# Performance work log

Hardware: AMD Instinct MI355X
Metric: run time of the kernel (lower is better)

The kernel has to match this reference:

```python
import jax, jax.numpy as jnp
import numpy as np

D_MODEL = 256
D_AUDIO = 256
W2V_DIM = 768
LIB_DIM = 93
N_LAYERS = 4
D_STATE = 16
D_CONV = 4
EXPAND = 2
D_INNER = EXPAND * D_MODEL  # 512
DT_RANK = (D_MODEL + 15) // 16  # 16
B, L = 8, 1024


def _silu(x):
    return x * jax.nn.sigmoid(x)


def _layernorm(x, g, b):
    mu = jnp.mean(x, axis=-1, keepdims=True)
    var = jnp.mean((x - mu) ** 2, axis=-1, keepdims=True)
    return (x - mu) * jax.lax.rsqrt(var + 1e-5) * g + b


def _mamba(x, in_W, conv_W, conv_b, xproj_W, dt_W, dt_b, A_log, D_vec, out_W):
    # x: [B, L, d_model]
    xz = jnp.einsum('bld,ed->ble', x, in_W)          # [B, L, 2*d_inner]
    xc, z = jnp.split(xz, 2, axis=-1)
    # causal depthwise conv1d over time
    u = jnp.swapaxes(xc, 1, 2)                        # [B, d_inner, L]
    u = jax.lax.conv_general_dilated(
        u, conv_W[:, None, :], (1,), [(D_CONV - 1, 0)],
        dimension_numbers=('NCH', 'OIH', 'NCH'), feature_group_count=D_INNER)
    xc = _silu(jnp.swapaxes(u, 1, 2) + conv_b)        # [B, L, d_inner]
    dbl = jnp.einsum('bld,ed->ble', xc, xproj_W)      # [B, L, dt_rank+2*d_state]
    dt, Bm, Cm = jnp.split(dbl, [DT_RANK, DT_RANK + D_STATE], axis=-1)
    dt = jax.nn.softplus(jnp.einsum('blr,dr->bld', dt, dt_W) + dt_b)  # [B, L, d_inner]
    A = -jnp.exp(A_log)                               # [d_inner, d_state]

    def step(h, inp):
        dt_t, x_t, B_t, C_t = inp                     # [B,d_inner],[B,d_inner],[B,S],[B,S]
        dA = jnp.exp(dt_t[..., None] * A)             # [B, d_inner, S]
        h = h * dA + (dt_t * x_t)[..., None] * B_t[:, None, :]
        y = jnp.einsum('bds,bs->bd', h, C_t)
        return h, y

    h0 = jnp.zeros((x.shape[0], D_INNER, D_STATE), x.dtype)
    xs = (jnp.swapaxes(dt, 0, 1), jnp.swapaxes(xc, 0, 1),
          jnp.swapaxes(Bm, 0, 1), jnp.swapaxes(Cm, 0, 1))
    _, ys = jax.lax.scan(step, h0, xs)                # ys: [L, B, d_inner]
    y = jnp.swapaxes(ys, 0, 1) + xc * D_vec
    y = y * _silu(z)
    return jnp.einsum('bld,ed->ble', y, out_W)


def setup_inputs() -> dict:
    key = jax.random.key(0)
    ks = jax.random.split(key, 24)

    def g(k, shape, scale):
        return (jax.random.normal(k, shape, dtype=jnp.float32) * scale)

    inp = {}
    inp['wav2vec_feat'] = jax.random.normal(ks[0], (B, L, W2V_DIM), dtype=jnp.float32)
    inp['librosa_feat'] = jax.random.normal(ks[1], (B, L, LIB_DIM), dtype=jnp.float32)
    inp['w2v_W'] = g(ks[2], (D_AUDIO, W2V_DIM), W2V_DIM ** -0.5)
    inp['w2v_b'] = jnp.zeros((D_AUDIO,), jnp.float32)
    inp['lib_W'] = g(ks[3], (D_AUDIO, LIB_DIM), LIB_DIM ** -0.5)
    inp['lib_b'] = jnp.zeros((D_AUDIO,), jnp.float32)
    inp['fuse_W'] = g(ks[4], (D_MODEL, 2 * D_AUDIO), (2 * D_AUDIO) ** -0.5)
    inp['fuse_b'] = jnp.zeros((D_MODEL,), jnp.float32)
    inp['proj_W'] = g(ks[5], (D_MODEL, D_MODEL), D_MODEL ** -0.5)
    inp['proj_b'] = jnp.zeros((D_MODEL,), jnp.float32)
    # stacked per-layer Mamba params, leading dim = N_LAYERS
    inp['ln_g'] = jnp.ones((N_LAYERS, D_MODEL), jnp.float32)
    inp['ln_b'] = jnp.zeros((N_LAYERS, D_MODEL), jnp.float32)
    inp['in_W'] = g(ks[6], (N_LAYERS, 2 * D_INNER, D_MODEL), D_MODEL ** -0.5)
    inp['conv_W'] = g(ks[7], (N_LAYERS, D_INNER, D_CONV), D_CONV ** -0.5)
    inp['conv_b'] = jnp.zeros((N_LAYERS, D_INNER), jnp.float32)
    inp['xproj_W'] = g(ks[8], (N_LAYERS, DT_RANK + 2 * D_STATE, D_INNER), D_INNER ** -0.5)
    inp['dt_W'] = g(ks[9], (N_LAYERS, D_INNER, DT_RANK), DT_RANK ** -0.5)
    inp['dt_b'] = jnp.full((N_LAYERS, D_INNER), -4.6, jnp.float32)  # softplus -> ~0.01
    A0 = jnp.log(jnp.arange(1, D_STATE + 1, dtype=jnp.float32))
    inp['A_log'] = jnp.broadcast_to(A0, (N_LAYERS, D_INNER, D_STATE)).copy()
    inp['D_vec'] = jnp.ones((N_LAYERS, D_INNER), jnp.float32)
    inp['out_W'] = g(ks[10], (N_LAYERS, D_MODEL, D_INNER), D_INNER ** -0.5)
    inp['fnorm_g'] = jnp.ones((D_MODEL,), jnp.float32)
    inp['fnorm_b'] = jnp.zeros((D_MODEL,), jnp.float32)
    return inp


def reference(wav2vec_feat, librosa_feat, w2v_W, w2v_b, lib_W, lib_b,
              fuse_W, fuse_b, proj_W, proj_b, ln_g, ln_b, in_W, conv_W, conv_b,
              xproj_W, dt_W, dt_b, A_log, D_vec, out_W, fnorm_g, fnorm_b):
    w = jnp.einsum('bld,ed->ble', wav2vec_feat, w2v_W) + w2v_b
    l = jnp.einsum('bld,ed->ble', librosa_feat, lib_W) + lib_b
    h = jnp.einsum('bld,ed->ble', jnp.concatenate([w, l], axis=-1), fuse_W) + fuse_b
    # MambaEncoder: proj -> blocks -> final norm
    h = jnp.einsum('bld,ed->ble', h, proj_W) + proj_b
    for i in range(N_LAYERS):
        h = h + _mamba(_layernorm(h, ln_g[i], ln_b[i]), in_W[i], conv_W[i],
                       conv_b[i], xproj_W[i], dt_W[i], dt_b[i], A_log[i],
                       D_vec[i], out_W[i])
    return _layernorm(h, fnorm_g, fnorm_b)
```

## Files before the change

kernel.cpp:

```cpp
#include <hip/hip_runtime.h>
#include <math.h>


#define CH 64
#define CT 16

typedef __attribute__((ext_vector_type(8))) short bfrag8;
typedef __attribute__((ext_vector_type(4))) float floatx4;

__device__ __forceinline__ float silu_f(float x) { return x / (1.f + __expf(-x)); }
__device__ __forceinline__ unsigned short f2bf(float x) {
    union { float f; unsigned int u; } c; c.f = x;
    unsigned int r = (c.u + 0x7fffu + ((c.u >> 16) & 1u)) >> 16;
    return (unsigned short)r;
}
__device__ __forceinline__ float bf2f(unsigned short u) {
    union { unsigned int u; float f; } c; c.u = ((unsigned int)u) << 16; return c.f;
}
__device__ __forceinline__ floatx4 exp4(floatx4 x) {
    floatx4 r;
    r[0] = __expf(x[0]); r[1] = __expf(x[1]); r[2] = __expf(x[2]); r[3] = __expf(x[3]);
    return r;
}

#define NJOBS 10
struct CvtJobs {
    const float* src[NJOBS];
    unsigned short* dst[NJOBS];
    int n_src[NJOBS];
    int n_tot[NJOBS];
    int start_blk[NJOBS + 1];
};
__global__ void conv_bf16_multi(CvtJobs J)
{
    int blk = blockIdx.x;
    int job = 0;
    while (job + 1 < NJOBS && blk >= J.start_blk[job + 1]) job++;
    int i = (blk - J.start_blk[job]) * 1024 + threadIdx.x * 4;
    if (i >= J.n_tot[job]) return;
    const float* src = J.src[job];
    unsigned short* dst = J.dst[job];
    int ns = J.n_src[job];
    if (i + 3 < ns) {
        float4 v = *(const float4*)(src + i);
        dst[i] = f2bf(v.x); dst[i+1] = f2bf(v.y); dst[i+2] = f2bf(v.z); dst[i+3] = f2bf(v.w);
    } else {
#pragma unroll
        for (int j = 0; j < 4; j++) dst[i+j] = (i+j < ns) ? f2bf(src[i+j]) : (unsigned short)0;
    }
}

__global__ void pad_bf16_kernel(const float* __restrict__ src, unsigned short* __restrict__ dst,
                                int rows, int cs, int cd)
{
    int i = blockIdx.x * 256 + threadIdx.x;
    if (i >= rows * cd) return;
    int row = i / cd, c = i - row * cd;
    dst[i] = (c < cs) ? f2bf(src[row * cs + c]) : (unsigned short)0;
}

template<int RM, int RN>
__global__ __launch_bounds__(64)
void dmfma_gemm(const unsigned short* __restrict__ A, int lda,
                const unsigned short* __restrict__ W, int ldw,
                int K, const float* __restrict__ bias, const float* __restrict__ Cin,
                float* __restrict__ Cf32, unsigned short* __restrict__ Cbf16,
                int N, int ldc, int act)
{
    int lane = threadIdx.x;
    int lm = lane & 15, qk = lane >> 4;
    int m0 = blockIdx.y * (16 * RM);
    int n0 = blockIdx.x * (16 * RN);

    const unsigned short* Ab = A + (size_t)(m0 + lm) * lda + qk * 8;
    const unsigned short* Wb = W + (size_t)(n0 + lm) * ldw + qk * 8;

    floatx4 acc[RM][RN];
#pragma unroll
    for (int i = 0; i < RM; i++)
#pragma unroll
        for (int j = 0; j < RN; j++) acc[i][j] = (floatx4){0.f, 0.f, 0.f, 0.f};

    bfrag8 af[RM], wf[RN];
#pragma unroll
    for (int i = 0; i < RM; i++) af[i] = *(const bfrag8*)(Ab + (size_t)i * 16 * lda);
#pragma unroll
    for (int j = 0; j < RN; j++) wf[j] = *(const bfrag8*)(Wb + (size_t)j * 16 * ldw);

    for (int k0 = 32; k0 < K; k0 += 32) {
        bfrag8 afn[RM], wfn[RN];
#pragma unroll
        for (int i = 0; i < RM; i++) afn[i] = *(const bfrag8*)(Ab + (size_t)i * 16 * lda + k0);
#pragma unroll
        for (int j = 0; j < RN; j++) wfn[j] = *(const bfrag8*)(Wb + (size_t)j * 16 * ldw + k0);
#pragma unroll
        for (int i = 0; i < RM; i++)
#pragma unroll
            for (int j = 0; j < RN; j++)
                acc[i][j] = __builtin_amdgcn_mfma_f32_16x16x32_bf16(af[i], wf[j], acc[i][j], 0, 0, 0);
#pragma unroll
        for (int i = 0; i < RM; i++) af[i] = afn[i];
#pragma unroll
        for (int j = 0; j < RN; j++) wf[j] = wfn[j];
    }
#pragma unroll
    for (int i = 0; i < RM; i++)
#pragma unroll
        for (int j = 0; j < RN; j++)
            acc[i][j] = __builtin_amdgcn_mfma_f32_16x16x32_bf16(af[i], wf[j], acc[i][j], 0, 0, 0);

#pragma unroll
    for (int i = 0; i < RM; i++) {
        int mrow = m0 + i * 16 + qk * 4;
#pragma unroll
        for (int j = 0; j < RN; j++) {
            int n = n0 + j * 16 + lm;
            if (n < N) {
#pragma unroll
                for (int r = 0; r < 4; r++) {
                    float v = acc[i][j][r];
                    size_t o = (size_t)(mrow + r) * ldc + n;
                    if (bias) v += bias[n];
                    if (act == 1) v = fmaxf(v, 0.f) + log1pf(__expf(-fabsf(v)));
                    if (Cin) v += Cin[o];
                    if (Cf32) Cf32[o] = v;
                    if (Cbf16) Cbf16[o] = f2bf(v);
                }
            }
        }
    }
}

__global__ void ln_kernel(const float* __restrict__ x, const float* __restrict__ g,
                          const float* __restrict__ b, float* __restrict__ yf,
                          unsigned short* __restrict__ ybf)
{
    int row = blockIdx.x * 4 + (threadIdx.x >> 6);
    int lane = threadIdx.x & 63;
    size_t o = (size_t)row * 256 + lane * 4;
    floatx4 v = *(const floatx4*)(x + o);
    float s1 = v[0] + v[1] + v[2] + v[3];
    float s2 = v[0]*v[0] + v[1]*v[1] + v[2]*v[2] + v[3]*v[3];
#pragma unroll
    for (int off = 1; off < 64; off <<= 1) {
        s1 += __shfl_xor(s1, off);
        s2 += __shfl_xor(s2, off);
    }
    float mu = s1 * (1.f / 256.f);
    float var = s2 * (1.f / 256.f) - mu * mu;
    float rs = rsqrtf(var + 1e-5f);
    floatx4 gv = *(const floatx4*)(g + lane * 4);
    floatx4 bv = *(const floatx4*)(b + lane * 4);
    floatx4 out = (v - mu) * rs * gv + bv;
    if (yf) *(floatx4*)(yf + o) = out;
    if (ybf) {
        ushort4 pk;
        pk.x = f2bf(out[0]); pk.y = f2bf(out[1]); pk.z = f2bf(out[2]); pk.w = f2bf(out[3]);
        *(ushort4*)(ybf + o) = pk;
    }
}

__global__ void conv_silu_kernel(const unsigned short* __restrict__ xz, const float* __restrict__ cw,
                                 const float* __restrict__ cb, unsigned short* __restrict__ xc)
{
    int idx = blockIdx.x * 256 + threadIdx.x;
    int d4 = (idx & 127) << 2;
    int bt = idx >> 7;
    int t = bt & 1023;
    floatx4 acc = *(const floatx4*)(cb + d4);
    floatx4 w0 = *(const floatx4*)(cw + d4 * 4);
    floatx4 w1 = *(const floatx4*)(cw + d4 * 4 + 4);
    floatx4 w2 = *(const floatx4*)(cw + d4 * 4 + 8);
    floatx4 w3 = *(const floatx4*)(cw + d4 * 4 + 12);
#pragma unroll
    for (int j = 0; j < 4; j++) {
        int tt = t + j - 3;
        if (tt >= 0) {
            ushort4 v = *(const ushort4*)(xz + (size_t)(bt + j - 3) * 1024 + d4);
            acc[0] += bf2f(v.x) * w0[j];
            acc[1] += bf2f(v.y) * w1[j];
            acc[2] += bf2f(v.z) * w2[j];
            acc[3] += bf2f(v.w) * w3[j];
        }
    }
    ushort4 o;
    o.x = f2bf(silu_f(acc[0])); o.y = f2bf(silu_f(acc[1]));
    o.z = f2bf(silu_f(acc[2])); o.w = f2bf(silu_f(acc[3]));
    *(ushort4*)(xc + (size_t)bt * 512 + d4) = o;
}

__global__ __launch_bounds__(256, 4)
void scan_chunk_kernel(const unsigned short* __restrict__ xc, const float* __restrict__ dbl,
                       const unsigned short* __restrict__ dtb, const float* __restrict__ A_log,
                       float* __restrict__ dtsums, float* __restrict__ Hbuf)
{
    int bi = blockIdx.x;
    int dgrp = bi & 1;
    int chunk = (bi >> 1) & (CH - 1);
    int b = bi >> 7;
    int d = dgrp * 256 + threadIdx.x;

    floatx4 a0 = -exp4(*(const floatx4*)(A_log + d * 16));
    floatx4 a1 = -exp4(*(const floatx4*)(A_log + d * 16 + 4));
    floatx4 a2 = -exp4(*(const floatx4*)(A_log + d * 16 + 8));
    floatx4 a3 = -exp4(*(const floatx4*)(A_log + d * 16 + 12));

    floatx4 z4 = (floatx4){0.f, 0.f, 0.f, 0.f};
    floatx4 h0 = z4, h1 = z4, h2 = z4, h3 = z4;
    float dtsum = 0.f;

    size_t rbt = (size_t)b * 1024 + chunk * CT;
    float dt_v = bf2f(dtb[rbt * 512 + d]);
    float x_v  = bf2f(xc[rbt * 512 + d]);
    const float* row = dbl + rbt * 48;
    floatx4 B0 = *(const floatx4*)(row + 16);
    floatx4 B1 = *(const floatx4*)(row + 20);
    floatx4 B2 = *(const floatx4*)(row + 24);
    floatx4 B3 = *(const floatx4*)(row + 28);

    for (int t = 0; t < CT - 1; t++) {
        size_t r2 = rbt + 1;
        float dt_n = bf2f(dtb[r2 * 512 + d]);
        float x_n  = bf2f(xc[r2 * 512 + d]);
        const float* rown = dbl + r2 * 48;
        floatx4 Bn0 = *(const floatx4*)(rown + 16);
        floatx4 Bn1 = *(const floatx4*)(rown + 20);
        floatx4 Bn2 = *(const floatx4*)(rown + 24);
        floatx4 Bn3 = *(const floatx4*)(rown + 28);

        float dtx = dt_v * x_v;
        dtsum += dt_v;
        floatx4 dA;
        dA = exp4(dt_v * a0); h0 = h0 * dA + dtx * B0;
        dA = exp4(dt_v * a1); h1 = h1 * dA + dtx * B1;
        dA = exp4(dt_v * a2); h2 = h2 * dA + dtx * B2;
        dA = exp4(dt_v * a3); h3 = h3 * dA + dtx * B3;

        dt_v = dt_n; x_v = x_n;
        B0 = Bn0; B1 = Bn1; B2 = Bn2; B3 = Bn3;
        rbt = r2;
    }
    {
        float dtx = dt_v * x_v;
        dtsum += dt_v;
        floatx4 dA;
        dA = exp4(dt_v * a0); h0 = h0 * dA + dtx * B0;
        dA = exp4(dt_v * a1); h1 = h1 * dA + dtx * B1;
        dA = exp4(dt_v * a2); h2 = h2 * dA + dtx * B2;
        dA = exp4(dt_v * a3); h3 = h3 * dA + dtx * B3;
    }
    size_t base = (size_t)chunk * 65536 + ((b * 512 + d) * 16);
    *(floatx4*)&Hbuf[base]      = h0;
    *(floatx4*)&Hbuf[base + 4]  = h1;
    *(floatx4*)&Hbuf[base + 8]  = h2;
    *(floatx4*)&Hbuf[base + 12] = h3;
    dtsums[chunk * 4096 + b * 512 + d] = dtsum;
}

__global__ void scan_carry_kernel(const float* __restrict__ dtsums, const float* __restrict__ A_log,
                                  float* __restrict__ Hbuf)
{
    int ch = blockIdx.x * 256 + threadIdx.x;
    int s = ch & 15;
    int bd = ch >> 4;
    int d = bd & 511;
    float a = -__expf(A_log[d * 16 + s]);
    float h = 0.f;
#pragma unroll 8
    for (int c = 0; c < CH; c++) {
        float hl = Hbuf[(size_t)c * 65536 + ch];
        float P = __expf(dtsums[c * 4096 + bd] * a);
        Hbuf[(size_t)c * 65536 + ch] = h;
        h = fmaf(P, h, hl);
    }
}

__global__ __launch_bounds__(256, 4)
void scan_final_kernel(const unsigned short* __restrict__ xc, const float* __restrict__ dbl,
                       const unsigned short* __restrict__ dtb, const unsigned short* __restrict__ xz,
                       const float* __restrict__ A_log, const float* __restrict__ Dvec,
                       const float* __restrict__ Hbuf, unsigned short* __restrict__ y)
{
    int bi = blockIdx.x;
    int dgrp = bi & 1;
    int chunk = (bi >> 1) & (CH - 1);
    int b = bi >> 7;
    int d = dgrp * 256 + threadIdx.x;

    floatx4 a0 = -exp4(*(const floatx4*)(A_log + d * 16));
    floatx4 a1 = -exp4(*(const floatx4*)(A_log + d * 16 + 4));
    floatx4 a2 = -exp4(*(const floatx4*)(A_log + d * 16 + 8));
    floatx4 a3 = -exp4(*(const floatx4*)(A_log + d * 16 + 12));
    float dcoef = Dvec[d];

    size_t base = (size_t)chunk * 65536 + ((b * 512 + d) * 16);
    floatx4 h0 = *(const floatx4*)&Hbuf[base];
    floatx4 h1 = *(const floatx4*)&Hbuf[base + 4];
    floatx4 h2 = *(const floatx4*)&Hbuf[base + 8];
    floatx4 h3 = *(const floatx4*)&Hbuf[base + 12];

    size_t rbt = (size_t)b * 1024 + chunk * CT;
    float dt_v = bf2f(dtb[rbt * 512 + d]);
    float x_v  = bf2f(xc[rbt * 512 + d]);
    float z_v  = bf2f(xz[rbt * 1024 + 512 + d]);
    const float* row = dbl + rbt * 48;
    floatx4 B0 = *(const floatx4*)(row + 16);
    floatx4 B1 = *(const floatx4*)(row + 20);
    floatx4 B2 = *(const floatx4*)(row + 24);
    floatx4 B3 = *(const floatx4*)(row + 28);

    for (int t = 0; t < CT - 1; t++) {
        size_t r2 = rbt + 1;
        float dt_n = bf2f(dtb[r2 * 512 + d]);
        float x_n  = bf2f(xc[r2 * 512 + d]);
        float z_n  = bf2f(xz[r2 * 1024 + 512 + d]);
        const float* rown = dbl + r2 * 48;
        floatx4 Bn0 = *(const floatx4*)(rown + 16);
        floatx4 Bn1 = *(const floatx4*)(rown + 20);
        floatx4 Bn2 = *(const floatx4*)(rown + 24);
        floatx4 Bn3 = *(const floatx4*)(rown + 28);

        float dtx = dt_v * x_v;
        floatx4 dA;
        dA = exp4(dt_v * a0); h0 = h0 * dA + dtx * B0;
        dA = exp4(dt_v * a1); h1 = h1 * dA + dtx * B1;
        dA = exp4(dt_v * a2); h2 = h2 * dA + dtx * B2;
        dA = exp4(dt_v * a3); h3 = h3 * dA + dtx * B3;
        floatx4 C0 = *(const floatx4*)(row + 32);
        floatx4 C1 = *(const floatx4*)(row + 36);
        floatx4 C2 = *(const floatx4*)(row + 40);
        floatx4 C3 = *(const floatx4*)(row + 44);
        floatx4 yv = h0 * C0 + h1 * C1 + h2 * C2 + h3 * C3;
        float yacc = yv[0] + yv[1] + yv[2] + yv[3];
        y[rbt * 512 + d] = f2bf((yacc + x_v * dcoef) * silu_f(z_v));

        dt_v = dt_n; x_v = x_n; z_v = z_n;
        B0 = Bn0; B1 = Bn1; B2 = Bn2; B3 = Bn3;
        row = rown; rbt = r2;
    }
    {
        float dtx = dt_v * x_v;
        floatx4 dA;
        dA = exp4(dt_v * a0); h0 = h0 * dA + dtx * B0;
        dA = exp4(dt_v * a1); h1 = h1 * dA + dtx * B1;
        dA = exp4(dt_v * a2); h2 = h2 * dA + dtx * B2;
        dA = exp4(dt_v * a3); h3 = h3 * dA + dtx * B3;
        floatx4 C0 = *(const floatx4*)(row + 32);
        floatx4 C1 = *(const floatx4*)(row + 36);
        floatx4 C2 = *(const floatx4*)(row + 40);
        floatx4 C3 = *(const floatx4*)(row + 44);
        floatx4 yv = h0 * C0 + h1 * C1 + h2 * C2 + h3 * C3;
        float yacc = yv[0] + yv[1] + yv[2] + yv[3];
        y[rbt * 512 + d] = f2bf((yacc + x_v * dcoef) * silu_f(z_v));
    }
}

extern "C" void kernel_launch(void* const* d_in, const int* in_sizes, int n_in,
                              void* d_out, int out_size, void* d_ws, size_t ws_size,
                              hipStream_t stream)
{
    const float* wav     = (const float*)d_in[0];
    const float* lib     = (const float*)d_in[1];
    const float* w2v_W   = (const float*)d_in[2];
    const float* w2v_b   = (const float*)d_in[3];
    const float* lib_W   = (const float*)d_in[4];
    const float* lib_b   = (const float*)d_in[5];
    const float* fuse_W  = (const float*)d_in[6];
    const float* fuse_b  = (const float*)d_in[7];
    const float* proj_W  = (const float*)d_in[8];
    const float* proj_b  = (const float*)d_in[9];
    const float* ln_g    = (const float*)d_in[10];
    const float* ln_b    = (const float*)d_in[11];
    const float* in_W    = (const float*)d_in[12];
    const float* conv_W  = (const float*)d_in[13];
    const float* conv_b  = (const float*)d_in[14];
    const float* xproj_W = (const float*)d_in[15];
    const float* dt_W    = (const float*)d_in[16];
    const float* dt_b    = (const float*)d_in[17];
    const float* A_log   = (const float*)d_in[18];
    const float* D_vec   = (const float*)d_in[19];
    const float* out_W   = (const float*)d_in[20];
    const float* fnorm_g = (const float*)d_in[21];
    const float* fnorm_b = (const float*)d_in[22];

    char* p = (char*)d_ws;
    float* hbuf = (float*)p;             p += 8192 * 256 * 4;
    unsigned short* xz_bf = (unsigned short*)p; p += (size_t)8192 * 1024 * 2;
    float* dblb = (float*)p;             p += 8192 * 48 * 4;
    unsigned short* dbl_bf = (unsigned short*)p; p += 8192 * 48 * 2;
    float* dtsums = (float*)p;           p += (size_t)CH * 4096 * 4;
    float* Hbuf = (float*)p;             p += (size_t)CH * 65536 * 4;
    unsigned short* xln_bf = (unsigned short*)p; p += 8192 * 256 * 2;
    unsigned short* xcb_bf = (unsigned short*)p; p += 8192 * 512 * 2;
    unsigned short* dtb_bf = (unsigned short*)p; p += 8192 * 512 * 2;
    unsigned short* yb_bf  = (unsigned short*)p; p += 8192 * 512 * 2;
    unsigned short* w2vWb  = (unsigned short*)p; p += 256 * 768 * 2;
    unsigned short* fuseWb = (unsigned short*)p; p += 256 * 512 * 2;
    unsigned short* projWb = (unsigned short*)p; p += 256 * 256 * 2;
    unsigned short* inWb   = (unsigned short*)p; p += 4 * 1024 * 256 * 2;
    unsigned short* xprojWb= (unsigned short*)p; p += 4 * 64 * 512 * 2;
    unsigned short* outWb  = (unsigned short*)p; p += 4 * 256 * 512 * 2;
    unsigned short* dtWb   = (unsigned short*)p; p += 4 * 512 * 32 * 2;
    unsigned short* lib_bf = (unsigned short*)p; p += 8192 * 96 * 2;
    unsigned short* libWb  = (unsigned short*)p; p += 256 * 96 * 2;
    unsigned short* wav_bf  = xcb_bf;
    unsigned short* cat_bf  = yb_bf;
    unsigned short* fuse_bf = xln_bf;

    dim3 blk(256);
    dim3 wblk(64);

    CvtJobs J;
    const float* srcs[NJOBS] = { wav, w2v_W, fuse_W, proj_W, in_W, out_W,
                                 xproj_W, xproj_W + 24576, xproj_W + 49152, xproj_W + 73728 };
    unsigned short* dsts[NJOBS] = { wav_bf, w2vWb, fuseWb, projWb, inWb, outWb,
                                    xprojWb, xprojWb + 32768, xprojWb + 65536, xprojWb + 98304 };
    int nsrc[NJOBS] = { 6291456, 196608, 131072, 65536, 1048576, 524288,
                        24576, 24576, 24576, 24576 };
    int ntot[NJOBS] = { 6291456, 196608, 131072, 65536, 1048576, 524288,
                        32768, 32768, 32768, 32768 };
    int sb = 0;
    for (int j = 0; j < NJOBS; j++) {
        J.src[j] = srcs[j]; J.dst[j] = dsts[j]; J.n_src[j] = nsrc[j]; J.n_tot[j] = ntot[j];
        J.start_blk[j] = sb; sb += ntot[j] / 1024;
    }
    J.start_blk[NJOBS] = sb;
    conv_bf16_multi<<<sb, blk, 0, stream>>>(J);
    pad_bf16_kernel<<<(8192 * 96 + 255) / 256, blk, 0, stream>>>(lib, lib_bf, 8192, 93, 96);
    pad_bf16_kernel<<<(256 * 96 + 255) / 256, blk, 0, stream>>>(lib_W, libWb, 256, 93, 96);
    pad_bf16_kernel<<<(2048 * 32 + 255) / 256, blk, 0, stream>>>(dt_W, dtWb, 2048, 16, 32);

    dmfma_gemm<2,2><<<dim3(8, 256), wblk, 0, stream>>>(wav_bf, 768, w2vWb, 768, 768, w2v_b,
                                                       nullptr, nullptr, cat_bf, 256, 512, 0);
    dmfma_gemm<2,2><<<dim3(8, 256), wblk, 0, stream>>>(lib_bf, 96, libWb, 96, 96, lib_b,
                                                       nullptr, nullptr, cat_bf + 256, 256, 512, 0);
    dmfma_gemm<2,2><<<dim3(8, 256), wblk, 0, stream>>>(cat_bf, 512, fuseWb, 512, 512, fuse_b,
                                                       nullptr, nullptr, fuse_bf, 256, 256, 0);
    dmfma_gemm<2,2><<<dim3(8, 256), wblk, 0, stream>>>(fuse_bf, 256, projWb, 256, 256, proj_b,
                                                       nullptr, hbuf, nullptr, 256, 256, 0);

    for (int i = 0; i < 4; i++) {
        ln_kernel<<<2048, blk, 0, stream>>>(hbuf, ln_g + i * 256, ln_b + i * 256, nullptr, xln_bf);
        dmfma_gemm<2,4><<<dim3(16, 256), wblk, 0, stream>>>(xln_bf, 256, inWb + (size_t)i * 262144, 256,
                                                            256, nullptr, nullptr, nullptr, xz_bf, 1024, 1024, 0);
        conv_silu_kernel<<<4096, blk, 0, stream>>>(xz_bf, conv_W + i * 2048, conv_b + i * 512, xcb_bf);
        dmfma_gemm<1,2><<<dim3(2, 512), wblk, 0, stream>>>(xcb_bf, 512, xprojWb + (size_t)i * 32768, 512,
                                                           512, nullptr, nullptr, dblb, dbl_bf, 48, 48, 0);
        dmfma_gemm<2,4><<<dim3(8, 256), wblk, 0, stream>>>(dbl_bf, 48, dtWb + (size_t)i * 16384, 32,
                                                           32, dt_b + i * 512, nullptr, nullptr, dtb_bf, 512, 512, 1);
        scan_chunk_kernel<<<1024, blk, 0, stream>>>(xcb_bf, dblb, dtb_bf, A_log + i * 8192,
                                                    dtsums, Hbuf);
        scan_carry_kernel<<<256, blk, 0, stream>>>(dtsums, A_log + i * 8192, Hbuf);
        scan_final_kernel<<<1024, blk, 0, stream>>>(xcb_bf, dblb, dtb_bf, xz_bf, A_log + i * 8192,
                                                    D_vec + i * 512, Hbuf, yb_bf);
        dmfma_gemm<2,2><<<dim3(8, 256), wblk, 0, stream>>>(yb_bf, 512, outWb + (size_t)i * 131072, 512,
                                                           512, nullptr, hbuf, hbuf, nullptr, 256, 256, 0);
    }

    ln_kernel<<<2048, blk, 0, stream>>>(hbuf, fnorm_g, fnorm_b, (float*)d_out, nullptr);
}
```

Measured before the change: 775.2 us.

## Fold dt projection into x_proj weights and split scan into local+correction passes

Precomputes the product of dt_W and the dt rows of xproj_W so a single GEMM over K=512 produces softplus(dt) and the B/C columns directly. This removes the separate rank-16 dt GEMM and the intermediate bf16 dbl buffer. The chunked scan now emits partial outputs in the first pass. The final pass no longer reruns the recurrence; it adds a carried-state correction using cumulative decay exp(S*A). This trades a full recurrence replay for an extra fp32 ypart buffer round trip and a larger composed GEMM (N=544), and rounds the composed weights to bf16.

```diff
diff --git a/kernel.cpp b/kernel.cpp
--- a/kernel.cpp
+++ b/kernel.cpp
@@ -23,11 +23,10 @@
     return r;
 }
 
-#define NJOBS 10
+#define NJOBS 6
 struct CvtJobs {
     const float* src[NJOBS];
     unsigned short* dst[NJOBS];
-    int n_src[NJOBS];
     int n_tot[NJOBS];
     int start_blk[NJOBS + 1];
 };
@@ -40,14 +39,8 @@
     if (i >= J.n_tot[job]) return;
     const float* src = J.src[job];
     unsigned short* dst = J.dst[job];
-    int ns = J.n_src[job];
-    if (i + 3 < ns) {
-        float4 v = *(const float4*)(src + i);
-        dst[i] = f2bf(v.x); dst[i+1] = f2bf(v.y); dst[i+2] = f2bf(v.z); dst[i+3] = f2bf(v.w);
-    } else {
-#pragma unroll
-        for (int j = 0; j < 4; j++) dst[i+j] = (i+j < ns) ? f2bf(src[i+j]) : (unsigned short)0;
-    }
+    float4 v = *(const float4*)(src + i);
+    dst[i] = f2bf(v.x); dst[i+1] = f2bf(v.y); dst[i+2] = f2bf(v.z); dst[i+3] = f2bf(v.w);
 }
 
 __global__ void pad_bf16_kernel(const float* __restrict__ src, unsigned short* __restrict__ dst,
@@ -57,6 +50,26 @@
     if (i >= rows * cd) return;
     int row = i / cd, c = i - row * cd;
     dst[i] = (c < cs) ? f2bf(src[row * cs + c]) : (unsigned short)0;
+}
+
+__global__ void compose_xpdt(const float* __restrict__ dtW, const float* __restrict__ xprojW,
+                             unsigned short* __restrict__ dst)
+{
+    int idx = blockIdx.x * 256 + threadIdx.x;
+    int l = idx / (544 * 512);
+    int rem = idx - l * (544 * 512);
+    int n = rem >> 9, k = rem & 511;
+    const float* xp = xprojW + l * 48 * 512;
+    float v;
+    if (n < 512) {
+        const float* w = dtW + l * 512 * 16 + n * 16;
+        v = 0.f;
+#pragma unroll
+        for (int r = 0; r < 16; r++) v = fmaf(w[r], xp[r * 512 + k], v);
+    } else {
+        v = xp[(16 + (n - 512)) * 512 + k];
+    }
+    dst[l * (544 * 512) + n * 512 + k] = f2bf(v);
 }
 
 template<int RM, int RN>
@@ -65,7 +78,7 @@
                 const unsigned short* __restrict__ W, int ldw,
                 int K, const float* __restrict__ bias, const float* __restrict__ Cin,
                 float* __restrict__ Cf32, unsigned short* __restrict__ Cbf16,
-                int N, int ldc, int act)
+                int N, int ldc)
 {
     int lane = threadIdx.x;
     int lm = lane & 15, qk = lane >> 4;
@@ -121,10 +134,79 @@
                     float v = acc[i][j][r];
                     size_t o = (size_t)(mrow + r) * ldc + n;
                     if (bias) v += bias[n];
-                    if (act == 1) v = fmaxf(v, 0.f) + log1pf(__expf(-fabsf(v)));
                     if (Cin) v += Cin[o];
                     if (Cf32) Cf32[o] = v;
                     if (Cbf16) Cbf16[o] = f2bf(v);
+                }
+            }
+        }
+    }
+}
+
+__global__ __launch_bounds__(64)
+void xproj_dt_gemm(const unsigned short* __restrict__ A, const unsigned short* __restrict__ W,
+                   const float* __restrict__ dt_bias, unsigned short* __restrict__ dtb,
+                   float* __restrict__ bc)
+{
+    const int K = 512;
+    int lane = threadIdx.x;
+    int lm = lane & 15, qk = lane >> 4;
+    int m0 = blockIdx.y * 32;
+    int n0 = blockIdx.x * 32;
+
+    const unsigned short* Ab = A + (size_t)(m0 + lm) * K + qk * 8;
+    const unsigned short* Wb = W + (size_t)(n0 + lm) * K + qk * 8;
+
+    floatx4 acc[2][2];
+#pragma unroll
+    for (int i = 0; i < 2; i++)
+#pragma unroll
+        for (int j = 0; j < 2; j++) acc[i][j] = (floatx4){0.f, 0.f, 0.f, 0.f};
+
+    bfrag8 af[2], wf[2];
+#pragma unroll
+    for (int i = 0; i < 2; i++) af[i] = *(const bfrag8*)(Ab + (size_t)i * 16 * K);
+#pragma unroll
+    for (int j = 0; j < 2; j++) wf[j] = *(const bfrag8*)(Wb + (size_t)j * 16 * K);
+
+    for (int k0 = 32; k0 < K; k0 += 32) {
+        bfrag8 afn[2], wfn[2];
+#pragma unroll
+        for (int i = 0; i < 2; i++) afn[i] = *(const bfrag8*)(Ab + (size_t)i * 16 * K + k0);
+#pragma unroll
+        for (int j = 0; j < 2; j++) wfn[j] = *(const bfrag8*)(Wb + (size_t)j * 16 * K + k0);
+#pragma unroll
+        for (int i = 0; i < 2; i++)
+#pragma unroll
+            for (int j = 0; j < 2; j++)
+                acc[i][j] = __builtin_amdgcn_mfma_f32_16x16x32_bf16(af[i], wf[j], acc[i][j], 0, 0, 0);
+#pragma unroll
+        for (int i = 0; i < 2; i++) af[i] = afn[i];
+#pragma unroll
+        for (int j = 0; j < 2; j++) wf[j] = wfn[j];
+    }
+#pragma unroll
+    for (int i = 0; i < 2; i++)
+#pragma unroll
+        for (int j = 0; j < 2; j++)
+            acc[i][j] = __builtin_amdgcn_mfma_f32_16x16x32_bf16(af[i], wf[j], acc[i][j], 0, 0, 0);
+
+#pragma unroll
+    for (int i = 0; i < 2; i++) {
+        int mrow = m0 + i * 16 + qk * 4;
+#pragma unroll
+        for (int j = 0; j < 2; j++) {
+            int n = n0 + j * 16 + lm;
+#pragma unroll
+            for (int r = 0; r < 4; r++) {
+                float v = acc[i][j][r];
+                int m = mrow + r;
+                if (n < 512) {
+                    v += dt_bias[n];
+                    v = fmaxf(v, 0.f) + log1pf(__expf(-fabsf(v)));
+                    dtb[(size_t)m * 512 + n] = f2bf(v);
+                } else {
+                    bc[(size_t)m * 32 + (n - 512)] = v;
                 }
             }
         }
@@ -190,9 +272,11 @@
 }
 
 __global__ __launch_bounds__(256, 4)
-void scan_chunk_kernel(const unsigned short* __restrict__ xc, const float* __restrict__ dbl,
+void scan_local_kernel(const unsigned short* __restrict__ xc, const float* __restrict__ bc,
                        const unsigned short* __restrict__ dtb, const float* __restrict__ A_log,
-                       float* __restrict__ dtsums, float* __restrict__ Hbuf)
+                       const float* __restrict__ Dvec,
+                       float* __restrict__ dtsums, float* __restrict__ Hbuf,
+                       float* __restrict__ ypart)
 {
     int bi = blockIdx.x;
     int dgrp = bi & 1;
@@ -204,6 +288,7 @@
     floatx4 a1 = -exp4(*(const floatx4*)(A_log + d * 16 + 4));
     floatx4 a2 = -exp4(*(const floatx4*)(A_log + d * 16 + 8));
     floatx4 a3 = -exp4(*(const floatx4*)(A_log + d * 16 + 12));
+    float dcoef = Dvec[d];
 
     floatx4 z4 = (floatx4){0.f, 0.f, 0.f, 0.f};
     floatx4 h0 = z4, h1 = z4, h2 = z4, h3 = z4;
@@ -212,21 +297,21 @@
     size_t rbt = (size_t)b * 1024 + chunk * CT;
     float dt_v = bf2f(dtb[rbt * 512 + d]);
     float x_v  = bf2f(xc[rbt * 512 + d]);
-    const float* row = dbl + rbt * 48;
-    floatx4 B0 = *(const floatx4*)(row + 16);
-    floatx4 B1 = *(const floatx4*)(row + 20);
-    floatx4 B2 = *(const floatx4*)(row + 24);
-    floatx4 B3 = *(const floatx4*)(row + 28);
+    const float* row = bc + rbt * 32;
+    floatx4 B0 = *(const floatx4*)(row);
+    floatx4 B1 = *(const floatx4*)(row + 4);
+    floatx4 B2 = *(const floatx4*)(row + 8);
+    floatx4 B3 = *(const floatx4*)(row + 12);
 
     for (int t = 0; t < CT - 1; t++) {
         size_t r2 = rbt + 1;
         float dt_n = bf2f(dtb[r2 * 512 + d]);
         float x_n  = bf2f(xc[r2 * 512 + d]);
-        const float* rown = dbl + r2 * 48;
-        floatx4 Bn0 = *(const floatx4*)(rown + 16);
-        floatx4 Bn1 = *(const floatx4*)(rown + 20);
-        floatx4 Bn2 = *(const floatx4*)(rown + 24);
-        floatx4 Bn3 = *(const floatx4*)(rown + 28);
+        const float* rown = bc + r2 * 32;
+        floatx4 Bn0 = *(const floatx4*)(rown);
+        floatx4 Bn1 = *(const floatx4*)(rown + 4);
+        floatx4 Bn2 = *(const floatx4*)(rown + 8);
+        floatx4 Bn3 = *(const floatx4*)(rown + 12);
 
         float dtx = dt_v * x_v;
         dtsum += dt_v;
@@ -235,10 +320,16 @@
         dA = exp4(dt_v * a1); h1 = h1 * dA + dtx * B1;
         dA = exp4(dt_v * a2); h2 = h2 * dA + dtx * B2;
         dA = exp4(dt_v * a3); h3 = h3 * dA + dtx * B3;
+        floatx4 C0 = *(const floatx4*)(row + 16);
+        floatx4 C1 = *(const floatx4*)(row + 20);
+        floatx4 C2 = *(const floatx4*)(row + 24);
+        floatx4 C3 = *(const floatx4*)(row + 28);
+        floatx4 yv = h0 * C0 + h1 * C1 + h2 * C2 + h3 * C3;
+        ypart[rbt * 512 + d] = yv[0] + yv[1] + yv[2] + yv[3] + x_v * dcoef;
 
         dt_v = dt_n; x_v = x_n;
         B0 = Bn0; B1 = Bn1; B2 = Bn2; B3 = Bn3;
-        rbt = r2;
+        row = rown; rbt = r2;
     }
     {
         float dtx = dt_v * x_v;
@@ -248,6 +339,12 @@
         dA = exp4(dt_v * a1); h1 = h1 * dA + dtx * B1;
         dA = exp4(dt_v * a2); h2 = h2 * dA + dtx * B2;
         dA = exp4(dt_v * a3); h3 = h3 * dA + dtx * B3;
+        floatx4 C0 = *(const floatx4*)(row + 16);
+        floatx4 C1 = *(const floatx4*)(row + 20);
+        floatx4 C2 = *(const floatx4*)(row + 24);
+        floatx4 C3 = *(const floatx4*)(row + 28);
+        floatx4 yv = h0 * C0 + h1 * C1 + h2 * C2 + h3 * C3;
+        ypart[rbt * 512 + d] = yv[0] + yv[1] + yv[2] + yv[3] + x_v * dcoef;
     }
     size_t base = (size_t)chunk * 65536 + ((b * 512 + d) * 16);
     *(floatx4*)&Hbuf[base]      = h0;
@@ -276,10 +373,10 @@
 }
 
 __global__ __launch_bounds__(256, 4)
-void scan_final_kernel(const unsigned short* __restrict__ xc, const float* __restrict__ dbl,
-                       const unsigned short* __restrict__ dtb, const unsigned short* __restrict__ xz,
-                       const float* __restrict__ A_log, const float* __restrict__ Dvec,
-                       const float* __restrict__ Hbuf, unsigned short* __restrict__ y)
+void scan_corr_kernel(const unsigned short* __restrict__ dtb, const float* __restrict__ bc,
+                      const unsigned short* __restrict__ xz, const float* __restrict__ ypart,
+                      const float* __restrict__ A_log, const float* __restrict__ Hbuf,
+                      unsigned short* __restrict__ y)
 {
     int bi = blockIdx.x;
     int dgrp = bi & 1;
@@ -291,7 +388,6 @@
     floatx4 a1 = -exp4(*(const floatx4*)(A_log + d * 16 + 4));
     floatx4 a2 = -exp4(*(const floatx4*)(A_log + d * 16 + 8));
     floatx4 a3 = -exp4(*(const floatx4*)(A_log + d * 16 + 12));
-    float dcoef = Dvec[d];
 
     size_t base = (size_t)chunk * 65536 + ((b * 512 + d) * 16);
     floatx4 h0 = *(const floatx4*)&Hbuf[base];
@@ -299,59 +395,23 @@
     floatx4 h2 = *(const floatx4*)&Hbuf[base + 8];
     floatx4 h3 = *(const floatx4*)&Hbuf[base + 12];
 
+    float S = 0.f;
     size_t rbt = (size_t)b * 1024 + chunk * CT;
-    float dt_v = bf2f(dtb[rbt * 512 + d]);
-    float x_v  = bf2f(xc[rbt * 512 + d]);
-    float z_v  = bf2f(xz[rbt * 1024 + 512 + d]);
-    const float* row = dbl + rbt * 48;
-    floatx4 B0 = *(const floatx4*)(row + 16);
-    floatx4 B1 = *(const floatx4*)(row + 20);
-    floatx4 B2 = *(const floatx4*)(row + 24);
-    floatx4 B3 = *(const floatx4*)(row + 28);
-
-    for (int t = 0; t < CT - 1; t++) {
-        size_t r2 = rbt + 1;
-        float dt_n = bf2f(dtb[r2 * 512 + d]);
-        float x_n  = bf2f(xc[r2 * 512 + d]);
-        float z_n  = bf2f(xz[r2 * 1024 + 512 + d]);
-        const float* rown = dbl + r2 * 48;
-        floatx4 Bn0 = *(const floatx4*)(rown + 16);
-        floatx4 Bn1 = *(const floatx4*)(rown + 20);
-        floatx4 Bn2 = *(const floatx4*)(rown + 24);
-        floatx4 Bn3 = *(const floatx4*)(rown + 28);
-
-        float dtx = dt_v * x_v;
-        floatx4 dA;
-        dA = exp4(dt_v * a0); h0 = h0 * dA + dtx * B0;
-        dA = exp4(dt_v * a1); h1 = h1 * dA + dtx * B1;
-        dA = exp4(dt_v * a2); h2 = h2 * dA + dtx * B2;
-        dA = exp4(dt_v * a3); h3 = h3 * dA + dtx * B3;
-        floatx4 C0 = *(const floatx4*)(row + 32);
-        floatx4 C1 = *(const floatx4*)(row + 36);
-        floatx4 C2 = *(const floatx4*)(row + 40);
-        floatx4 C3 = *(const floatx4*)(row + 44);
-        floatx4 yv = h0 * C0 + h1 * C1 + h2 * C2 + h3 * C3;
-        float yacc = yv[0] + yv[1] + yv[2] + yv[3];
-        y[rbt * 512 + d] = f2bf((yacc + x_v * dcoef) * silu_f(z_v));
-
-        dt_v = dt_n; x_v = x_n; z_v = z_n;
-        B0 = Bn0; B1 = Bn1; B2 = Bn2; B3 = Bn3;
-        row = rown; rbt = r2;
-    }
-    {
-        float dtx = dt_v * x_v;
-        floatx4 dA;
-        dA = exp4(dt_v * a0); h0 = h0 * dA + dtx * B0;
-        dA = exp4(dt_v * a1); h1 = h1 * dA + dtx * B1;
-        dA = exp4(dt_v * a2); h2 = h2 * dA + dtx * B2;
-        dA = exp4(dt_v * a3); h3 = h3 * dA + dtx * B3;
-        floatx4 C0 = *(const floatx4*)(row + 32);
-        floatx4 C1 = *(const floatx4*)(row + 36);
-        floatx4 C2 = *(const floatx4*)(row + 40);
-        floatx4 C3 = *(const floatx4*)(row + 44);
-        floatx4 yv = h0 * C0 + h1 * C1 + h2 * C2 + h3 * C3;
-        float yacc = yv[0] + yv[1] + yv[2] + yv[3];
-        y[rbt * 512 + d] = f2bf((yacc + x_v * dcoef) * silu_f(z_v));
+#pragma unroll 4
+    for (int t = 0; t < CT; t++, rbt++) {
+        float dt_v = bf2f(dtb[rbt * 512 + d]);
+        S += dt_v;
+        const float* row = bc + rbt * 32;
+        floatx4 C0 = *(const floatx4*)(row + 16);
+        floatx4 C1 = *(const floatx4*)(row + 20);
+        floatx4 C2 = *(const floatx4*)(row + 24);
+        floatx4 C3 = *(const floatx4*)(row + 28);
+        floatx4 cv = (h0 * exp4(S * a0)) * C0 + (h1 * exp4(S * a1)) * C1
+                   + (h2 * exp4(S * a2)) * C2 + (h3 * exp4(S * a3)) * C3;
+        float corr = cv[0] + cv[1] + cv[2] + cv[3];
+        float yp = ypart[rbt * 512 + d];
+        float z  = bf2f(xz[rbt * 1024 + 512 + d]);
+        y[rbt * 512 + d] = f2bf((yp + corr) * silu_f(z));
     }
 }
 
@@ -386,10 +446,10 @@
     char* p = (char*)d_ws;
     float* hbuf = (float*)p;             p += 8192 * 256 * 4;
     unsigned short* xz_bf = (unsigned short*)p; p += (size_t)8192 * 1024 * 2;
-    float* dblb = (float*)p;             p += 8192 * 48 * 4;
-    unsigned short* dbl_bf = (unsigned short*)p; p += 8192 * 48 * 2;
+    float* dblb = (float*)p;             p += 8192 * 32 * 4;
     float* dtsums = (float*)p;           p += (size_t)CH * 4096 * 4;
     float* Hbuf = (float*)p;             p += (size_t)CH * 65536 * 4;
+    float* ypart = (float*)p;            p += (size_t)8192 * 512 * 4;
     unsigned short* xln_bf = (unsigned short*)p; p += 8192 * 256 * 2;
     unsigned short* xcb_bf = (unsigned short*)p; p += 8192 * 512 * 2;
     unsigned short* dtb_bf = (unsigned short*)p; p += 8192 * 512 * 2;
@@ -398,9 +458,8 @@
     unsigned short* fuseWb = (unsigned short*)p; p += 256 * 512 * 2;
     unsigned short* projWb = (unsigned short*)p; p += 256 * 256 * 2;
     unsigned short* inWb   = (unsigned short*)p; p += 4 * 1024 * 256 * 2;
-    unsigned short* xprojWb= (unsigned short*)p; p += 4 * 64 * 512 * 2;
     unsigned short* outWb  = (unsigned short*)p; p += 4 * 256 * 512 * 2;
-    unsigned short* dtWb   = (unsigned short*)p; p += 4 * 512 * 32 * 2;
+    unsigned short* xpdtWb = (unsigned short*)p; p += (size_t)4 * 544 * 512 * 2;
     unsigned short* lib_bf = (unsigned short*)p; p += 8192 * 96 * 2;
     unsigned short* libWb  = (unsigned short*)p; p += 256 * 96 * 2;
     unsigned short* wav_bf  = xcb_bf;
@@ -411,50 +470,43 @@
     dim3 wblk(64);
 
     CvtJobs J;
-    const float* srcs[NJOBS] = { wav, w2v_W, fuse_W, proj_W, in_W, out_W,
-                                 xproj_W, xproj_W + 24576, xproj_W + 49152, xproj_W + 73728 };
-    unsigned short* dsts[NJOBS] = { wav_bf, w2vWb, fuseWb, projWb, inWb, outWb,
-                                    xprojWb, xprojWb + 32768, xprojWb + 65536, xprojWb + 98304 };
-    int nsrc[NJOBS] = { 6291456, 196608, 131072, 65536, 1048576, 524288,
-                        24576, 24576, 24576, 24576 };
-    int ntot[NJOBS] = { 6291456, 196608, 131072, 65536, 1048576, 524288,
-                        32768, 32768, 32768, 32768 };
+    const float* srcs[NJOBS] = { wav, w2v_W, fuse_W, proj_W, in_W, out_W };
+    unsigned short* dsts[NJOBS] = { wav_bf, w2vWb, fuseWb, projWb, inWb, outWb };
+    int ntot[NJOBS] = { 6291456, 196608, 131072, 65536, 1048576, 524288 };
     int sb = 0;
     for (int j = 0; j < NJOBS; j++) {
-        J.src[j] = srcs[j]; J.dst[j] = dsts[j]; J.n_src[j] = nsrc[j]; J.n_tot[j] = ntot[j];
+        J.src[j] = srcs[j]; J.dst[j] = dsts[j]; J.n_tot[j] = ntot[j];
         J.start_blk[j] = sb; sb += ntot[j] / 1024;
     }
     J.start_blk[NJOBS] = sb;
     conv_bf16_multi<<<sb, blk, 0, stream>>>(J);
     pad_bf16_kernel<<<(8192 * 96 + 255) / 256, blk, 0, stream>>>(lib, lib_bf, 8192, 93, 96);
     pad_bf16_kernel<<<(256 * 96 + 255) / 256, blk, 0, stream>>>(lib_W, libWb, 256, 93, 96);
-    pad_bf16_kernel<<<(2048 * 32 + 255) / 256, blk, 0, stream>>>(dt_W, dtWb, 2048, 16, 32);
+    compose_xpdt<<<(4 * 544 * 512) / 256, blk, 0, stream>>>(dt_W, xproj_W, xpdtWb);
 
     dmfma_gemm<2,2><<<dim3(8, 256), wblk, 0, stream>>>(wav_bf, 768, w2vWb, 768, 768, w2v_b,
-                                                       nullptr, nullptr, cat_bf, 256, 512, 0);
+                                                       nullptr, nullptr, cat_bf, 256, 512);
     dmfma_gemm<2,2><<<dim3(8, 256), wblk, 0, stream>>>(lib_bf, 96, libWb, 96, 96, lib_b,
-                                                       nullptr, nullptr, cat_bf + 256, 256, 512, 0);
+                                                       nullptr, nullptr, cat_bf + 256, 256, 512);
     dmfma_gemm<2,2><<<dim3(8, 256), wblk, 0, stream>>>(cat_bf, 512, fuseWb, 512, 512, fuse_b,
-                                                       nullptr, nullptr, fuse_bf, 256, 256, 0);
+                                                       nullptr, nullptr, fuse_bf, 256, 256);
     dmfma_gemm<2,2><<<dim3(8, 256), wblk, 0, stream>>>(fuse_bf, 256, projWb, 256, 256, proj_b,
-                                                       nullptr, hbuf, nullptr, 256, 256, 0);
+                                                       nullptr, hbuf, nullptr, 256, 256);
 
     for (int i = 0; i < 4; i++) {
         ln_kernel<<<2048, blk, 0, stream>>>(hbuf, ln_g + i * 256, ln_b + i * 256, nullptr, xln_bf);
         dmfma_gemm<2,4><<<dim3(16, 256), wblk, 0, stream>>>(xln_bf, 256, inWb + (size_t)i * 262144, 256,
-                                                            256, nullptr, nullptr, nullptr, xz_bf, 1024, 1024, 0);
+                                                            256, nullptr, nullptr, nullptr, xz_bf, 1024, 1024);
         conv_silu_kernel<<<4096, blk, 0, stream>>>(xz_bf, conv_W + i * 2048, conv_b + i * 512, xcb_bf);
-        dmfma_gemm<1,2><<<dim3(2, 512), wblk, 0, stream>>>(xcb_bf, 512, xprojWb + (size_t)i * 32768, 512,
-                                                           512, nullptr, nullptr, dblb, dbl_bf, 48, 48, 0);
-        dmfma_gemm<2,4><<<dim3(8, 256), wblk, 0, stream>>>(dbl_bf, 48, dtWb + (size_t)i * 16384, 32,
-                                                           32, dt_b + i * 512, nullptr, nullptr, dtb_bf, 512, 512, 1);
-        scan_chunk_kernel<<<1024, blk, 0, stream>>>(xcb_bf, dblb, dtb_bf, A_log + i * 8192,
-                                                    dtsums, Hbuf);
+        xproj_dt_gemm<<<dim3(17, 256), wblk, 0, stream>>>(xcb_bf, xpdtWb + (size_t)i * 544 * 512,
+                                                          dt_b + i * 512, dtb_bf, dblb);
+        scan_local_kernel<<<1024, blk, 0, stream>>>(xcb_bf, dblb, dtb_bf, A_log + i * 8192,
+                                                    D_vec + i * 512, dtsums, Hbuf, ypart);
         scan_carry_kernel<<<256, blk, 0, stream>>>(dtsums, A_log + i * 8192, Hbuf);
-        scan_final_kernel<<<1024, blk, 0, stream>>>(xcb_bf, dblb, dtb_bf, xz_bf, A_log + i * 8192,
-                                                    D_vec + i * 512, Hbuf, yb_bf);
+        scan_corr_kernel<<<1024, blk, 0, stream>>>(dtb_bf, dblb, xz_bf, ypart,
+                                                   A_log + i * 8192, Hbuf, yb_bf);
         dmfma_gemm<2,2><<<dim3(8, 256), wblk, 0, stream>>>(yb_bf, 512, outWb + (size_t)i * 131072, 512,
-                                                           512, nullptr, hbuf, hbuf, nullptr, 256, 256, 0);
+                                                           512, nullptr, hbuf, hbuf, nullptr, 256, 256);
     }
 
     ln_kernel<<<2048, blk, 0, stream>>>(hbuf, fnorm_g, fnorm_b, (float*)d_out, nullptr);
```

Result: slower. 826.1 us (+6.6%).

## Compute local scan outputs in chunk pass and apply carry-in as correction

Applied to the files above, without the earlier changes.

The chunked selective scan now emits the chunk-local output (including the D skip term) in the first pass, storing it in a new fp32 buffer. The final pass no longer reruns the recurrence. It adds the carried-in state's contribution as h_in·exp(cumsum(dt)·A)·C and applies the SiLU gate. This removes the second sequential recurrence, at the cost of writing and rereading an fp32 partial-output buffer and recomputing the exponentials in the correction pass. The xproj weight padding also moves from the multi-job converter to the pad kernel, which simplifies the converter.

```diff
diff --git a/kernel.cpp b/kernel.cpp
--- a/kernel.cpp
+++ b/kernel.cpp
@@ -23,11 +23,10 @@
     return r;
 }
 
-#define NJOBS 10
+#define NJOBS 6
 struct CvtJobs {
     const float* src[NJOBS];
     unsigned short* dst[NJOBS];
-    int n_src[NJOBS];
     int n_tot[NJOBS];
     int start_blk[NJOBS + 1];
 };
@@ -40,14 +39,8 @@
     if (i >= J.n_tot[job]) return;
     const float* src = J.src[job];
     unsigned short* dst = J.dst[job];
-    int ns = J.n_src[job];
-    if (i + 3 < ns) {
-        float4 v = *(const float4*)(src + i);
-        dst[i] = f2bf(v.x); dst[i+1] = f2bf(v.y); dst[i+2] = f2bf(v.z); dst[i+3] = f2bf(v.w);
-    } else {
-#pragma unroll
-        for (int j = 0; j < 4; j++) dst[i+j] = (i+j < ns) ? f2bf(src[i+j]) : (unsigned short)0;
-    }
+    float4 v = *(const float4*)(src + i);
+    dst[i] = f2bf(v.x); dst[i+1] = f2bf(v.y); dst[i+2] = f2bf(v.z); dst[i+3] = f2bf(v.w);
 }
 
 __global__ void pad_bf16_kernel(const float* __restrict__ src, unsigned short* __restrict__ dst,
@@ -190,9 +183,11 @@
 }
 
 __global__ __launch_bounds__(256, 4)
-void scan_chunk_kernel(const unsigned short* __restrict__ xc, const float* __restrict__ dbl,
+void scan_local_kernel(const unsigned short* __restrict__ xc, const float* __restrict__ dbl,
                        const unsigned short* __restrict__ dtb, const float* __restrict__ A_log,
-                       float* __restrict__ dtsums, float* __restrict__ Hbuf)
+                       const float* __restrict__ Dvec,
+                       float* __restrict__ dtsums, float* __restrict__ Hbuf,
+                       float* __restrict__ ypart)
 {
     int bi = blockIdx.x;
     int dgrp = bi & 1;
@@ -204,6 +199,7 @@
     floatx4 a1 = -exp4(*(const floatx4*)(A_log + d * 16 + 4));
     floatx4 a2 = -exp4(*(const floatx4*)(A_log + d * 16 + 8));
     floatx4 a3 = -exp4(*(const floatx4*)(A_log + d * 16 + 12));
+    float dcoef = Dvec[d];
 
     floatx4 z4 = (floatx4){0.f, 0.f, 0.f, 0.f};
     floatx4 h0 = z4, h1 = z4, h2 = z4, h3 = z4;
@@ -235,10 +231,16 @@
         dA = exp4(dt_v * a1); h1 = h1 * dA + dtx * B1;
         dA = exp4(dt_v * a2); h2 = h2 * dA + dtx * B2;
         dA = exp4(dt_v * a3); h3 = h3 * dA + dtx * B3;
+        floatx4 C0 = *(const floatx4*)(row + 32);
+        floatx4 C1 = *(const floatx4*)(row + 36);
+        floatx4 C2 = *(const floatx4*)(row + 40);
+        floatx4 C3 = *(const floatx4*)(row + 44);
+        floatx4 yv = h0 * C0 + h1 * C1 + h2 * C2 + h3 * C3;
+        ypart[rbt * 512 + d] = yv[0] + yv[1] + yv[2] + yv[3] + x_v * dcoef;
 
         dt_v = dt_n; x_v = x_n;
         B0 = Bn0; B1 = Bn1; B2 = Bn2; B3 = Bn3;
-        rbt = r2;
+        row = rown; rbt = r2;
     }
     {
         float dtx = dt_v * x_v;
@@ -248,6 +250,12 @@
         dA = exp4(dt_v * a1); h1 = h1 * dA + dtx * B1;
         dA = exp4(dt_v * a2); h2 = h2 * dA + dtx * B2;
         dA = exp4(dt_v * a3); h3 = h3 * dA + dtx * B3;
+        floatx4 C0 = *(const floatx4*)(row + 32);
+        floatx4 C1 = *(const floatx4*)(row + 36);
+        floatx4 C2 = *(const floatx4*)(row + 40);
+        floatx4 C3 = *(const floatx4*)(row + 44);
+        floatx4 yv = h0 * C0 + h1 * C1 + h2 * C2 + h3 * C3;
+        ypart[rbt * 512 + d] = yv[0] + yv[1] + yv[2] + yv[3] + x_v * dcoef;
     }
     size_t base = (size_t)chunk * 65536 + ((b * 512 + d) * 16);
     *(floatx4*)&Hbuf[base]      = h0;
@@ -276,10 +284,10 @@
 }
 
 __global__ __launch_bounds__(256, 4)
-void scan_final_kernel(const unsigned short* __restrict__ xc, const float* __restrict__ dbl,
-                       const unsigned short* __restrict__ dtb, const unsigned short* __restrict__ xz,
-                       const float* __restrict__ A_log, const float* __restrict__ Dvec,
-                       const float* __restrict__ Hbuf, unsigned short* __restrict__ y)
+void scan_corr_kernel(const unsigned short* __restrict__ dtb, const float* __restrict__ dbl,
+                      const unsigned short* __restrict__ xz, const float* __restrict__ ypart,
+                      const float* __restrict__ A_log, const float* __restrict__ Hbuf,
+                      unsigned short* __restrict__ y)
 {
     int bi = blockIdx.x;
     int dgrp = bi & 1;
@@ -291,7 +299,6 @@
     floatx4 a1 = -exp4(*(const floatx4*)(A_log + d * 16 + 4));
     floatx4 a2 = -exp4(*(const floatx4*)(A_log + d * 16 + 8));
     floatx4 a3 = -exp4(*(const floatx4*)(A_log + d * 16 + 12));
-    float dcoef = Dvec[d];
 
     size_t base = (size_t)chunk * 65536 + ((b * 512 + d) * 16);
     floatx4 h0 = *(const floatx4*)&Hbuf[base];
@@ -299,59 +306,23 @@
     floatx4 h2 = *(const floatx4*)&Hbuf[base + 8];
     floatx4 h3 = *(const floatx4*)&Hbuf[base + 12];
 
+    float S = 0.f;
     size_t rbt = (size_t)b * 1024 + chunk * CT;
-    float dt_v = bf2f(dtb[rbt * 512 + d]);
-    float x_v  = bf2f(xc[rbt * 512 + d]);
-    float z_v  = bf2f(xz[rbt * 1024 + 512 + d]);
-    const float* row = dbl + rbt * 48;
-    floatx4 B0 = *(const floatx4*)(row + 16);
-    floatx4 B1 = *(const floatx4*)(row + 20);
-    floatx4 B2 = *(const floatx4*)(row + 24);
-    floatx4 B3 = *(const floatx4*)(row + 28);
-
-    for (int t = 0; t < CT - 1; t++) {
-        size_t r2 = rbt + 1;
-        float dt_n = bf2f(dtb[r2 * 512 + d]);
-        float x_n  = bf2f(xc[r2 * 512 + d]);
-        float z_n  = bf2f(xz[r2 * 1024 + 512 + d]);
-        const float* rown = dbl + r2 * 48;
-        floatx4 Bn0 = *(const floatx4*)(rown + 16);
-        floatx4 Bn1 = *(const floatx4*)(rown + 20);
-        floatx4 Bn2 = *(const floatx4*)(rown + 24);
-        floatx4 Bn3 = *(const floatx4*)(rown + 28);
-
-        float dtx = dt_v * x_v;
-        floatx4 dA;
-        dA = exp4(dt_v * a0); h0 = h0 * dA + dtx * B0;
-        dA = exp4(dt_v * a1); h1 = h1 * dA + dtx * B1;
-        dA = exp4(dt_v * a2); h2 = h2 * dA + dtx * B2;
-        dA = exp4(dt_v * a3); h3 = h3 * dA + dtx * B3;
+#pragma unroll 4
+    for (int t = 0; t < CT; t++, rbt++) {
+        float dt_v = bf2f(dtb[rbt * 512 + d]);
+        S += dt_v;
+        const float* row = dbl + rbt * 48;
         floatx4 C0 = *(const floatx4*)(row + 32);
         floatx4 C1 = *(const floatx4*)(row + 36);
         floatx4 C2 = *(const floatx4*)(row + 40);
         floatx4 C3 = *(const floatx4*)(row + 44);
-        floatx4 yv = h0 * C0 + h1 * C1 + h2 * C2 + h3 * C3;
-        float yacc = yv[0] + yv[1] + yv[2] + yv[3];
-        y[rbt * 512 + d] = f2bf((yacc + x_v * dcoef) * silu_f(z_v));
-
-        dt_v = dt_n; x_v = x_n; z_v = z_n;
-        B0 = Bn0; B1 = Bn1; B2 = Bn2; B3 = Bn3;
-        row = rown; rbt = r2;
-    }
-    {
-        float dtx = dt_v * x_v;
-        floatx4 dA;
-        dA = exp4(dt_v * a0); h0 = h0 * dA + dtx * B0;
-        dA = exp4(dt_v * a1); h1 = h1 * dA + dtx * B1;
-        dA = exp4(dt_v * a2); h2 = h2 * dA + dtx * B2;
-        dA = exp4(dt_v * a3); h3 = h3 * dA + dtx * B3;
-        floatx4 C0 = *(const floatx4*)(row + 32);
-        floatx4 C1 = *(const floatx4*)(row + 36);
-        floatx4 C2 = *(const floatx4*)(row + 40);
-        floatx4 C3 = *(const floatx4*)(row + 44);
-        floatx4 yv = h0 * C0 + h1 * C1 + h2 * C2 + h3 * C3;
-        float yacc = yv[0] + yv[1] + yv[2] + yv[3];
-        y[rbt * 512 + d] = f2bf((yacc + x_v * dcoef) * silu_f(z_v));
+        floatx4 cv = (h0 * exp4(S * a0)) * C0 + (h1 * exp4(S * a1)) * C1
+                   + (h2 * exp4(S * a2)) * C2 + (h3 * exp4(S * a3)) * C3;
+        float corr = cv[0] + cv[1] + cv[2] + cv[3];
+        float yp = ypart[rbt * 512 + d];
+        float z  = bf2f(xz[rbt * 1024 + 512 + d]);
+        y[rbt * 512 + d] = f2bf((yp + corr) * silu_f(z));
     }
 }
 
@@ -390,6 +361,7 @@
     unsigned short* dbl_bf = (unsigned short*)p; p += 8192 * 48 * 2;
     float* dtsums = (float*)p;           p += (size_t)CH * 4096 * 4;
     float* Hbuf = (float*)p;             p += (size_t)CH * 65536 * 4;
+    float* ypart = (float*)p;            p += (size_t)8192 * 512 * 4;
     unsigned short* xln_bf = (unsigned short*)p; p += 8192 * 256 * 2;
     unsigned short* xcb_bf = (unsigned short*)p; p += 8192 * 512 * 2;
     unsigned short* dtb_bf = (unsigned short*)p; p += 8192 * 512 * 2;
@@ -398,8 +370,8 @@
     unsigned short* fuseWb = (unsigned short*)p; p += 256 * 512 * 2;
     unsigned short* projWb = (unsigned short*)p; p += 256 * 256 * 2;
     unsigned short* inWb   = (unsigned short*)p; p += 4 * 1024 * 256 * 2;
+    unsigned short* outWb  = (unsigned short*)p; p += 4 * 256 * 512 * 2;
     unsigned short* xprojWb= (unsigned short*)p; p += 4 * 64 * 512 * 2;
-    unsigned short* outWb  = (unsigned short*)p; p += 4 * 256 * 512 * 2;
     unsigned short* dtWb   = (unsigned short*)p; p += 4 * 512 * 32 * 2;
     unsigned short* lib_bf = (unsigned short*)p; p += 8192 * 96 * 2;
     unsigned short* libWb  = (unsigned short*)p; p += 256 * 96 * 2;
@@ -411,23 +383,19 @@
     dim3 wblk(64);
 
     CvtJobs J;
-    const float* srcs[NJOBS] = { wav, w2v_W, fuse_W, proj_W, in_W, out_W,
-                                 xproj_W, xproj_W + 24576, xproj_W + 49152, xproj_W + 73728 };
-    unsigned short* dsts[NJOBS] = { wav_bf, w2vWb, fuseWb, projWb, inWb, outWb,
-                                    xprojWb, xprojWb + 32768, xprojWb + 65536, xprojWb + 98304 };
-    int nsrc[NJOBS] = { 6291456, 196608, 131072, 65536, 1048576, 524288,
-                        24576, 24576, 24576, 24576 };
-    int ntot[NJOBS] = { 6291456, 196608, 131072, 65536, 1048576, 524288,
-                        32768, 32768, 32768, 32768 };
+    const float* srcs[NJOBS] = { wav, w2v_W, fuse_W, proj_W, in_W, out_W };
+    unsigned short* dsts[NJOBS] = { wav_bf, w2vWb, fuseWb, projWb, inWb, outWb };
+    int ntot[NJOBS] = { 6291456, 196608, 131072, 65536, 1048576, 524288 };
     int sb = 0;
     for (int j = 0; j < NJOBS; j++) {
-        J.src[j] = srcs[j]; J.dst[j] = dsts[j]; J.n_src[j] = nsrc[j]; J.n_tot[j] = ntot[j];
+        J.src[j] = srcs[j]; J.dst[j] = dsts[j]; J.n_tot[j] = ntot[j];
         J.start_blk[j] = sb; sb += ntot[j] / 1024;
     }
     J.start_blk[NJOBS] = sb;
     conv_bf16_multi<<<sb, blk, 0, stream>>>(J);
     pad_bf16_kernel<<<(8192 * 96 + 255) / 256, blk, 0, stream>>>(lib, lib_bf, 8192, 93, 96);
     pad_bf16_kernel<<<(256 * 96 + 255) / 256, blk, 0, stream>>>(lib_W, libWb, 256, 93, 96);
+    pad_bf16_kernel<<<(4 * 32768 + 255) / 256, blk, 0, stream>>>(xproj_W, xprojWb, 4, 24576, 32768);
     pad_bf16_kernel<<<(2048 * 32 + 255) / 256, blk, 0, stream>>>(dt_W, dtWb, 2048, 16, 32);
 
     dmfma_gemm<2,2><<<dim3(8, 256), wblk, 0, stream>>>(wav_bf, 768, w2vWb, 768, 768, w2v_b,
@@ -448,11 +416,11 @@
                                                            512, nullptr, nullptr, dblb, dbl_bf, 48, 48, 0);
         dmfma_gemm<2,4><<<dim3(8, 256), wblk, 0, stream>>>(dbl_bf, 48, dtWb + (size_t)i * 16384, 32,
                                                            32, dt_b + i * 512, nullptr, nullptr, dtb_bf, 512, 512, 1);
-        scan_chunk_kernel<<<1024, blk, 0, stream>>>(xcb_bf, dblb, dtb_bf, A_log + i * 8192,
-                                                    dtsums, Hbuf);
+        scan_local_kernel<<<1024, blk, 0, stream>>>(xcb_bf, dblb, dtb_bf, A_log + i * 8192,
+                                                    D_vec + i * 512, dtsums, Hbuf, ypart);
         scan_carry_kernel<<<256, blk, 0, stream>>>(dtsums, A_log + i * 8192, Hbuf);
-        scan_final_kernel<<<1024, blk, 0, stream>>>(xcb_bf, dblb, dtb_bf, xz_bf, A_log + i * 8192,
-                                                    D_vec + i * 512, Hbuf, yb_bf);
+        scan_corr_kernel<<<1024, blk, 0, stream>>>(dtb_bf, dblb, xz_bf, ypart,
+                                                   A_log + i * 8192, Hbuf, yb_bf);
         dmfma_gemm<2,2><<<dim3(8, 256), wblk, 0, stream>>>(yb_bf, 512, outWb + (size_t)i * 131072, 512,
                                                            512, nullptr, hbuf, hbuf, nullptr, 256, 256, 0);
     }
```

New measurement: 771.6 us. Within noise of the previous version (-0.5%).
